# Kernel tuning notes

Measured on AMD Instinct MI355X. Metric: run time of the kernel, lower is better.

## Reference

```python
import jax, jax.numpy as jnp
import numpy as np

B, N = 2, 6
H, W = 64, 64            # BEV grid
FH, FW = 32, 88          # camera feature map
DIM, FEAT_DIM = 128, 128
HEADS, DH = 4, 32
QW1, QW2 = 8, 8          # query window
KW1, KW2 = 4, 11         # key/val window
IMG_H, IMG_W = 224, 480
EPS = 1e-5


def _ln(t, g, b):
    m = t.mean(-1, keepdims=True)
    v = ((t - m) ** 2).mean(-1, keepdims=True)
    return (t - m) / jnp.sqrt(v + EPS) * g + b


def _bn_relu_conv(t, g, b, Wc):
    # eval-mode BatchNorm2d (running_mean=0, running_var=1) -> ReLU -> 1x1 conv
    y = jax.nn.relu(t / jnp.sqrt(1.0 + EPS) * g[:, None, None] + b[:, None, None])
    return jnp.einsum('oc,nchw->nohw', Wc, y)


def _normalize(t, axis):
    n = jnp.sqrt(jnp.sum(t * t, axis=axis, keepdims=True))
    return t / jnp.maximum(n, 1e-12)


def _win(t, w1, w2):
    # (..., X*w1, Y*w2, d) -> (..., X, Y, w1, w2, d)
    s = t.shape
    t = t.reshape(*s[:-3], s[-3] // w1, w1, s[-2] // w2, w2, s[-1])
    return jnp.swapaxes(t, -4, -3)


def _unwin(t):
    # (..., X, Y, w1, w2, d) -> (..., X*w1, Y*w2, d)
    s = t.shape
    return jnp.swapaxes(t, -4, -3).reshape(*s[:-5], s[-5] * s[-3], s[-4] * s[-2], s[-1])


def _gridwin(t, w1, w2):
    bb, nn, Ht, Wt, d = t.shape
    t = t.reshape(bb, nn, w1, Ht // w1, w2, Wt // w2, d)
    return t.transpose(0, 1, 3, 5, 2, 4, 6)  # (b, n, X, Y, w1, w2, d)


def _cross_win_attn(qw, kw, vw, ln_g, ln_b, Wqkv, bqkv, Wp, bp, skip):
    b, n, X, Y, w1, w2, d = qw.shape
    f1, f2 = kw.shape[4], kw.shape[5]
    L = X * Y
    q = qw.transpose(0, 2, 3, 1, 4, 5, 6).reshape(b, L, n * w1 * w2, d)
    k = kw.transpose(0, 2, 3, 1, 4, 5, 6).reshape(b, L, n * f1 * f2, d)
    v = vw.transpose(0, 2, 3, 1, 4, 5, 6).reshape(b, L, n * f1 * f2, d)
    q = _ln(q, ln_g[0], ln_b[0]) @ Wqkv[0] + bqkv[0]
    k = _ln(k, ln_g[1], ln_b[1]) @ Wqkv[1] + bqkv[1]
    v = _ln(v, ln_g[2], ln_b[2]) @ Wqkv[2] + bqkv[2]
    split = lambda t: t.reshape(*t.shape[:-1], HEADS, DH)  # head-major channel split
    q, k, v = split(q), split(k), split(v)
    att = jax.nn.softmax(DH ** -0.5 * jnp.einsum('blqhd,blkhd->bhlqk', q, k), axis=-1)
    o = jnp.einsum('bhlqk,blkhd->blqhd', att, v).reshape(b, L, n * w1 * w2, HEADS * DH)
    o = o @ Wp + bp
    o = o.reshape(b, X, Y, n, w1, w2, d).mean(3)  # mean over cameras
    return o + skip


def _forward(x, grid, feature, I_inv, E_inv,
             bn_fl_g, bn_fl_b, W_fl, bn_fp_g, bn_fp_b, W_fp,
             W_bev, b_bev, W_img, W_cam,
             attn_ln_g, attn_ln_b, attn_Wqkv, attn_bqkv, attn_Wp, attn_bp,
             pn_g, pn_b, Wma, bma, Wmb, bmb, post_g, post_b):
    b, n = feature.shape[:2]
    # image plane (buffer)
    xs = jnp.linspace(0.0, 1.0, FW) * IMG_W
    ys = jnp.linspace(0.0, 1.0, FH) * IMG_H
    gx, gy = jnp.meshgrid(xs, ys)  # (FH, FW) each
    plane = jnp.stack([gx, gy, jnp.ones_like(gx)], 0).reshape(3, FH * FW)
    # camera embedding from translation column of E_inv
    c = E_inv[..., -1]                                   # (b, n, 4)
    c_embed = jnp.einsum('oc,bnc->bno', W_cam, c)        # (b, n, dim)
    # unprojected rays
    cam = jnp.einsum('bnij,jk->bnik', I_inv, plane)      # (b, n, 3, HW)
    cam = jnp.concatenate([cam, jnp.ones_like(cam[:, :, :1])], 2)
    d = jnp.einsum('bnij,bnjk->bnik', E_inv, cam)        # (b, n, 4, HW)
    d_img = d.reshape(b, n, 4, FH, FW)
    d_embed = jnp.einsum('oc,bnchw->bnohw', W_img, d_img)
    img_embed = _normalize(d_embed - c_embed[..., None, None], axis=2)
    # BEV positional embedding
    w_embed = jnp.einsum('oc,chw->ohw', W_bev, grid[:2]) + b_bev[:, None, None]
    bev_embed = _normalize(w_embed[None, None] - c_embed[..., None, None], axis=2)  # (b,n,dim,H,W)
    feat = feature.reshape(b * n, FEAT_DIM, FH, FW)
    key_im = img_embed + _bn_relu_conv(feat, bn_fp_g, bn_fp_b, W_fp).reshape(b, n, DIM, FH, FW)
    val_im = _bn_relu_conv(feat, bn_fl_g, bn_fl_b, W_fl).reshape(b, n, DIM, FH, FW)
    query = bev_embed + x[:, None]                       # (b, n, dim, H, W)
    # channel-last
    q_im = query.transpose(0, 1, 3, 4, 2)
    k_im = key_im.transpose(0, 1, 3, 4, 2)
    v_im = val_im.transpose(0, 1, 3, 4, 2)
    x_im = x.transpose(0, 2, 3, 1)
    # stage 1: local windows
    qw = _win(q_im, QW1, QW2)
    kw = _win(k_im, KW1, KW2)
    vw = _win(v_im, KW1, KW2)
    o1 = _cross_win_attn(qw, kw, vw, attn_ln_g[0], attn_ln_b[0], attn_Wqkv[0],
                         attn_bqkv[0], attn_Wp[0], attn_bp[0], _win(x_im, QW1, QW2))
    q1 = _unwin(o1)                                      # (b, H, W, d)
    q1 = q1 + jax.nn.gelu(_ln(q1, pn_g[0], pn_b[0]) @ Wma[0] + bma[0], approximate=False) @ Wmb[0] + bmb[0]
    # stage 2: grid (swapped) windows
    qg = jnp.broadcast_to(q1[:, None], (b, n) + q1.shape[1:])
    o2 = _cross_win_attn(_win(qg, QW1, QW2), _gridwin(k_im, KW1, KW2), _gridwin(v_im, KW1, KW2),
                         attn_ln_g[1], attn_ln_b[1], attn_Wqkv[1], attn_bqkv[1],
                         attn_Wp[1], attn_bp[1], _win(q1, QW1, QW2))
    q2 = _unwin(o2)
    q2 = q2 + jax.nn.gelu(_ln(q2, pn_g[1], pn_b[1]) @ Wma[1] + bma[1], approximate=False) @ Wmb[1] + bmb[1]
    out = _ln(q2, post_g, post_b)
    return out.transpose(0, 3, 1, 2)                     # (b, dim, H, W)


def setup_inputs() -> dict:
    key = jax.random.key(0)
    ks = jax.random.split(key, 16)
    rn = lambda i, shape, sc=0.02: jax.random.normal(ks[i], shape, dtype=jnp.float32) * sc
    return {
        'index': 0,
        'x': jax.random.normal(ks[0], (B, DIM, H, W), dtype=jnp.float32),
        'grid': jax.random.normal(ks[1], (2, H, W), dtype=jnp.float32),
        'feature': jax.random.normal(ks[2], (B, N, FEAT_DIM, FH, FW), dtype=jnp.float32),
        'I_inv': jax.random.normal(ks[3], (B, N, 3, 3), dtype=jnp.float32),
        'E_inv': jax.random.normal(ks[4], (B, N, 4, 4), dtype=jnp.float32),
        'bn_fl_g': jnp.ones((FEAT_DIM,), jnp.float32), 'bn_fl_b': jnp.zeros((FEAT_DIM,), jnp.float32),
        'W_fl': rn(5, (DIM, FEAT_DIM)),
        'bn_fp_g': jnp.ones((FEAT_DIM,), jnp.float32), 'bn_fp_b': jnp.zeros((FEAT_DIM,), jnp.float32),
        'W_fp': rn(6, (DIM, FEAT_DIM)),
        'W_bev': rn(7, (DIM, 2)), 'b_bev': jnp.zeros((DIM,), jnp.float32),
        'W_img': rn(8, (DIM, 4)), 'W_cam': rn(9, (DIM, 4)),
        'attn_ln_g': jnp.ones((2, 3, DIM), jnp.float32), 'attn_ln_b': jnp.zeros((2, 3, DIM), jnp.float32),
        'attn_Wqkv': rn(10, (2, 3, DIM, HEADS * DH)), 'attn_bqkv': jnp.zeros((2, 3, HEADS * DH), jnp.float32),
        'attn_Wp': rn(11, (2, HEADS * DH, DIM)), 'attn_bp': jnp.zeros((2, DIM), jnp.float32),
        'pn_g': jnp.ones((2, DIM), jnp.float32), 'pn_b': jnp.zeros((2, DIM), jnp.float32),
        'Wma': rn(12, (2, DIM, 2 * DIM)), 'bma': jnp.zeros((2, 2 * DIM), jnp.float32),
        'Wmb': rn(13, (2, 2 * DIM, DIM)), 'bmb': jnp.zeros((2, DIM), jnp.float32),
        'post_g': jnp.ones((DIM,), jnp.float32), 'post_b': jnp.zeros((DIM,), jnp.float32),
    }


def reference(index, x, grid, feature, I_inv, E_inv,
              bn_fl_g, bn_fl_b, W_fl, bn_fp_g, bn_fp_b, W_fp,
              W_bev, b_bev, W_img, W_cam,
              attn_ln_g, attn_ln_b, attn_Wqkv, attn_bqkv, attn_Wp, attn_bp,
              pn_g, pn_b, Wma, bma, Wmb, bmb, post_g, post_b):
    del index  # grid for this index is passed directly
    return _forward(x, grid, feature, I_inv, E_inv,
                    bn_fl_g, bn_fl_b, W_fl, bn_fp_g, bn_fp_b, W_fp,
                    W_bev, b_bev, W_img, W_cam,
                    attn_ln_g, attn_ln_b, attn_Wqkv, attn_bqkv, attn_Wp, attn_bp,
                    pn_g, pn_b, Wma, bma, Wmb, bmb, post_g, post_b)
```

## Files before the change

### kernel.cpp

```cpp
#include <hip/hip_runtime.h>
#include <math.h>


typedef __attribute__((ext_vector_type(8))) short short8;
typedef __attribute__((ext_vector_type(4))) float f32x4;

__device__ __forceinline__ unsigned short f2bf(float f){
  union { float f; unsigned u; } v; v.f = f;
  unsigned r = v.u + 0x7FFF + ((v.u >> 16) & 1);
  return (unsigned short)(r >> 16);
}
__device__ __forceinline__ float bf2f(unsigned short h){
  union { unsigned u; float f; } v; v.u = ((unsigned)h) << 16; return v.f;
}
__device__ __forceinline__ void store_bf16x8(unsigned short* p, const float* v){
  union { short8 s8; unsigned short u[8]; } u;
  #pragma unroll
  for (int i=0;i<8;i++) u.u[i] = f2bf(v[i]);
  *(short8*)p = u.s8;
}

__device__ __forceinline__ float gelu_erf(float x){
  float z = x * 0.70710678118654752f;
  float a = fabsf(z);
  float t = 1.0f / fmaf(0.3275911f, a, 1.0f);
  float p = t*(0.254829592f + t*(-0.284496736f + t*(1.421413741f +
            t*(-1.453152027f + t*1.061405429f))));
  float er = 1.0f - p*__expf(-a*a);
  er = copysignf(er, z);
  return 0.5f * x * (1.0f + er);
}

__device__ __forceinline__ size_t remap_kv(int tok, int mode){
  int bn = tok / 2816; int p = tok - bn*2816;
  int b = bn / 6, n = bn - b*6;
  int i = p / 88, j = p - i*88;
  int l, t;
  if (mode == 1){
    int jw = j / 11;
    l = (i >> 2)*8 + jw;
    t = n*44 + (i & 3)*11 + (j - jw*11);
  } else {
    l = (i & 7)*8 + (j & 7);
    t = n*44 + (i >> 3)*11 + (j >> 3);
  }
  return (size_t)((b*64 + l)*264 + t);
}

__global__ __launch_bounds__(128) void k_prep(
    const float* __restrict__ qkv, const float* __restrict__ wp,
    const float* __restrict__ wma, const float* __restrict__ wmb,
    const float* __restrict__ wfl, const float* __restrict__ wfp,
    unsigned short* __restrict__ Wt,
    const float* __restrict__ Iinv, const float* __restrict__ Einv,
    const float* __restrict__ Wimg, const float* __restrict__ Wcam,
    unsigned short* __restrict__ K1h,
    const float* __restrict__ gridp, const float* __restrict__ Wbev,
    const float* __restrict__ bbev, const float* __restrict__ x,
    const float* __restrict__ lg, const float* __restrict__ lb,
    unsigned short* __restrict__ Qh){
  __shared__ float sx[128][9];
  int bid = blockIdx.x;
  if (bid < 64){
    const int sel[16]  = {0,0,0,0,0,0, 1,1, 2,2, 3,3,3,3, 4,5};
    const int soff[16] = {0,16384,32768,49152,65536,81920, 0,16384, 0,32768,
                          0,16384,32768,49152, 0,0};
    const int doff[16] = {0,16384,32768,49152,65536,81920, 98304,114688,
                          131072,163840, 196608,212992,229376,245760, 262144,278528};
    const int Ns[16]   = {128,128,128,128,128,128, 128,128, 256,256,
                          128,128,128,128, 128,128};
    const int trs[16]  = {1,1,1,1,1,1, 1,1, 1,1, 1,1,1,1, 0,0};
    int sg = bid >> 2, q = bid & 3;
    const float* srcs[6] = {qkv, wp, wma, wmb, wfl, wfp};
    const float* src = srcs[sel[sg]] + soff[sg];
    unsigned short* dst = Wt + doff[sg];
    int K = 128, N = Ns[sg];
    int quarter = (K*N) >> 2;
    for (int idx = q*quarter + threadIdx.x; idx < (q+1)*quarter; idx += 128){
      int n = idx / K, k = idx - n*K;
      float v = trs[sg] ? src[k*N + n] : src[idx];
      dst[idx] = f2bf(v);
    }
  } else if (bid < 4288){
    int tile = bid - 64;
    int bn = tile / 352; int p0 = (tile - bn*352)*8;
    int xid = threadIdx.x >> 4, part = threadIdx.x & 15;
    int p = p0 + xid;
    int i = p / 88, j = p - i*88;
    float xs = (float)j * (480.0f/87.0f);
    float ys = (float)i * (224.0f/31.0f);
    const float* I = Iinv + bn*9;
    const float* E = Einv + bn*16;
    float c0 = I[0]*xs + I[1]*ys + I[2];
    float c1 = I[3]*xs + I[4]*ys + I[5];
    float c2 = I[6]*xs + I[7]*ys + I[8];
    float d0 = E[0]*c0 + E[1]*c1 + E[2]*c2 + E[3];
    float d1 = E[4]*c0 + E[5]*c1 + E[6]*c2 + E[7];
    float d2 = E[8]*c0 + E[9]*c1 + E[10]*c2 + E[11];
    float d3 = E[12]*c0 + E[13]*c1 + E[14]*c2 + E[15];
    float v[8]; float sq = 0.f;
    #pragma unroll
    for (int k=0;k<8;k++){
      int o = part*8 + k;
      const float* W = Wimg + o*4;
      const float* Wc = Wcam + o*4;
      float de = W[0]*d0 + W[1]*d1 + W[2]*d2 + W[3]*d3;
      float ce = Wc[0]*E[3] + Wc[1]*E[7] + Wc[2]*E[11] + Wc[3]*E[15];
      float vv = de - ce;
      v[k] = vv; sq = fmaf(vv, vv, sq);
    }
    #pragma unroll
    for (int off=8; off>0; off>>=1) sq += __shfl_xor(sq, off, 16);
    float rn = 1.0f / fmaxf(sqrtf(sq), 1e-12f);
    float o8[8];
    #pragma unroll
    for (int k=0;k<8;k++) o8[k] = v[k]*rn;
    store_bf16x8(K1h + (size_t)(bn*2816 + p)*128 + part*8, o8);
  } else {
    int bid2 = bid - 4288;
    int b = bid2 >> 9; int pp0 = (bid2 & 511) << 3;
    {
      int cg = threadIdx.x >> 3, px = threadIdx.x & 7;
      #pragma unroll
      for (int i=0;i<8;i++){
        int c = cg + 16*i;
        sx[c][px] = x[(size_t)b*524288 + (size_t)c*4096 + pp0 + px];
      }
    }
    __syncthreads();
    int xid = threadIdx.x >> 4, part = threadIdx.x & 15;
    int pix = pp0 + xid;
    int h = pix >> 6, w = pix & 63;
    int l = (h>>3)*8 + (w>>3);
    int tq = (h&7)*8 + (w&7);
    float g0 = gridp[pix], g1 = gridp[4096 + pix];
    float we[8], xv[8];
    #pragma unroll
    for (int k=0;k<8;k++){
      int o = part*8 + k;
      we[k] = Wbev[o*2]*g0 + Wbev[o*2+1]*g1 + bbev[o];
      xv[k] = sx[part*8+k][xid];
    }
    for (int n=0; n<6; n++){
      const float* E = Einv + (b*6+n)*16;
      float v[8]; float sq = 0.f;
      #pragma unroll
      for (int k=0;k<8;k++){
        int o = part*8 + k;
        const float* Wc = Wcam + o*4;
        float ce = Wc[0]*E[3] + Wc[1]*E[7] + Wc[2]*E[11] + Wc[3]*E[15];
        float vv = we[k] - ce;
        v[k] = vv; sq = fmaf(vv, vv, sq);
      }
      #pragma unroll
      for (int off=8; off>0; off>>=1) sq += __shfl_xor(sq, off, 16);
      float rn = 1.0f / fmaxf(sqrtf(sq), 1e-12f);
      float q[8]; float s=0.f, s2=0.f;
      #pragma unroll
      for (int k=0;k<8;k++){
        q[k] = fmaf(v[k], rn, xv[k]);
        s += q[k]; s2 = fmaf(q[k], q[k], s2);
      }
      #pragma unroll
      for (int off=8; off>0; off>>=1){ s += __shfl_xor(s, off, 16); s2 += __shfl_xor(s2, off, 16); }
      float mean = s*(1.f/128.f);
      float rstd = rsqrtf(fmaxf(s2*(1.f/128.f) - mean*mean, 0.f) + 1e-5f);
      size_t row = (size_t)((b*64 + l)*384 + n*64 + tq);
      float o8[8];
      #pragma unroll
      for (int k=0;k<8;k++){
        int c = part*8 + k;
        o8[k] = fmaf((q[k]-mean)*rstd, lg[c], lb[c]);
      }
      store_bf16x8(Qh + row*128 + part*8, o8);
    }
  }
}

struct GArg {
  const unsigned short* Xh; const float* Xf; int ldx;
  const float* lg; const float* lb;
  const unsigned short* Wt; const float* bias;
  unsigned short* OUTH; int ldout; float oscale;
  int do_ln; int outmode; int conv;
};

template<int MT>
__global__ __launch_bounds__(256) void k_gemm3(GArg ga, GArg gb, GArg gc,
                                               int s1, int s2){
  constexpr int KP_ = 136;
  constexpr int MTILES = MT / 16;
  constexpr int TPR = 256 / MT;
  constexpr int KPT = 128 / TPR;
  __shared__ unsigned short sW[128*KP_];
  __shared__ unsigned short sA[MT*KP_];
  __shared__ float sg[128], sb[128], sbias[128];
  const int b0 = (int)blockIdx.x;
  const GArg g = (b0 < s1) ? ga : (b0 < s2) ? gb : gc;
  const int bid = (b0 < s1) ? b0 : (b0 < s2) ? b0 - s1 : b0 - s2;
  const int base = bid * MT;
  const int tid = threadIdx.x;
  for (int i = tid; i < 2048; i += 256){
    int n = i >> 4, k8 = (i & 15) << 3;
    *(short8*)&sW[n*KP_ + k8] = *(const short8*)(g.Wt + (size_t)n*128 + k8);
  }
  if (tid < 128){
    if (g.do_ln || g.conv){ sg[tid]=g.lg[tid]; sb[tid]=g.lb[tid]; }
    sbias[tid] = g.bias ? g.bias[tid] : 0.f;
  }
  const float RSQ = rsqrtf(1.0f + 1e-5f);
  if (g.conv){
    int prow = tid & 63, cseg = tid >> 6;
    int bn = base / 2816;
    int p = base - bn*2816 + prow;
    const float* fb = g.Xf + ((size_t)bn*128 + cseg*32)*2816 + p;
    #pragma unroll
    for (int i=0;i<32;i+=2){
      int c = cseg*32 + i;
      float t0 = fb[(size_t)i*2816] * RSQ;
      float t1 = fb[(size_t)(i+1)*2816] * RSQ;
      float y0 = fmaxf(fmaf(t0, sg[c],   sb[c]),   0.f);
      float y1 = fmaxf(fmaf(t1, sg[c+1], sb[c+1]), 0.f);
      unsigned u = (unsigned)f2bf(y0) | ((unsigned)f2bf(y1) << 16);
      *(unsigned*)&sA[prow*KP_ + c] = u;
    }
  } else {
    const int r = tid / TPR, part = tid % TPR;
    unsigned short* dst = sA + r*KP_ + part*KPT;
    float v[KPT];
    if (g.Xf){
      const float* src = g.Xf + (size_t)(base+r)*g.ldx + part*KPT;
      #pragma unroll
      for (int k=0;k<KPT;k+=4){
        float4 t = *(const float4*)(src + k);
        v[k]=t.x; v[k+1]=t.y; v[k+2]=t.z; v[k+3]=t.w;
      }
    } else {
      const unsigned short* src = g.Xh + (size_t)(base+r)*g.ldx + part*KPT;
      #pragma unroll
      for (int k=0;k<KPT;k+=8){
        union { short8 s; unsigned short u[8]; } t;
        t.s = *(const short8*)(src+k);
        #pragma unroll
        for (int i2=0;i2<8;i2++) v[k+i2] = bf2f(t.u[i2]);
      }
    }
    if (g.do_ln){
      float s=0.f, s2=0.f;
      #pragma unroll
      for (int k=0;k<KPT;k++){ s += v[k]; s2 = fmaf(v[k],v[k],s2); }
      #pragma unroll
      for (int off=TPR/2; off>0; off>>=1){
        s += __shfl_xor(s, off, TPR); s2 += __shfl_xor(s2, off, TPR);
      }
      float mean = s * (1.f/128.f);
      float rstd = rsqrtf(fmaxf(s2*(1.f/128.f) - mean*mean, 0.f) + 1e-5f);
      #pragma unroll
      for (int k=0;k<KPT;k++){
        int c = part*KPT + k;
        v[k] = fmaf((v[k]-mean)*rstd, sg[c], sb[c]);
      }
    }
    #pragma unroll
    for (int k=0;k<KPT;k+=8) store_bf16x8(dst+k, v+k);
  }
  __syncthreads();
  const int lane = tid & 63, wv = tid >> 6;
  const int lane15 = lane & 15, quad = lane >> 4;
  const int n0 = wv * 32;
  f32x4 acc[MTILES][2];
  #pragma unroll
  for (int mt=0; mt<MTILES; mt++){ acc[mt][0]=(f32x4)0.f; acc[mt][1]=(f32x4)0.f; }
  const unsigned short* aptr = sA + lane15*KP_ + quad*8;
  const unsigned short* bptr = sW + (size_t)(n0 + lane15)*KP_ + quad*8;
  #pragma unroll
  for (int kk=0; kk<4; kk++){
    short8 af[MTILES], bf2v[2];
    #pragma unroll
    for (int mt=0; mt<MTILES; mt++) af[mt] = *(const short8*)(aptr + mt*16*KP_ + kk*32);
    bf2v[0] = *(const short8*)(bptr + kk*32);
    bf2v[1] = *(const short8*)(bptr + 16*KP_ + kk*32);
    #pragma unroll
    for (int mt=0; mt<MTILES; mt++){
      acc[mt][0] = __builtin_amdgcn_mfma_f32_16x16x32_bf16(af[mt], bf2v[0], acc[mt][0], 0,0,0);
      acc[mt][1] = __builtin_amdgcn_mfma_f32_16x16x32_bf16(af[mt], bf2v[1], acc[mt][1], 0,0,0);
    }
  }
  __syncthreads();
  #pragma unroll
  for (int mt=0; mt<MTILES; mt++){
    #pragma unroll
    for (int nt=0; nt<2; nt++){
      int col = n0 + nt*16 + lane15;
      float bsv = sbias[col];
      #pragma unroll
      for (int r4=0; r4<4; r4++){
        int row = mt*16 + quad*4 + r4;
        float v = (acc[mt][nt][r4] + bsv) * g.oscale;
        if (g.outmode == 3)
          v += bf2f(g.OUTH[(size_t)(base+row)*g.ldout + col]);
        sA[row*KP_ + col] = f2bf(v);
      }
    }
  }
  __syncthreads();
  for (int i = tid; i < MT*16; i += 256){
    int row = i >> 4, seg = i & 15;
    int rrow = base + row;
    size_t orow = (g.outmode==1||g.outmode==2) ? remap_kv(rrow, g.outmode) : (size_t)rrow;
    *(short8*)(g.OUTH + orow*(size_t)g.ldout + seg*8) = *(const short8*)&sA[row*KP_ + seg*8];
  }
}

__global__ __launch_bounds__(256) void k_tail(
    const unsigned short* __restrict__ AOh,
    const float* __restrict__ skipf, int skipmode,
    const unsigned short* __restrict__ WtP, const float* __restrict__ abp,
    const float* __restrict__ png, const float* __restrict__ pnb,
    const unsigned short* __restrict__ WtMAa, const unsigned short* __restrict__ WtMAb,
    const float* __restrict__ bma,
    const unsigned short* __restrict__ WtMBa, const unsigned short* __restrict__ WtMBb,
    const float* __restrict__ bmb,
    float* __restrict__ Q1out,
    const float* __restrict__ postg, const float* __restrict__ postb,
    float* __restrict__ out){
  constexpr int KP_ = 136;
  __shared__ unsigned short sW[128*KP_];
  __shared__ unsigned short sX[32*KP_];
  __shared__ unsigned short sH1[32*KP_];
  __shared__ unsigned short sH2[32*KP_];
  __shared__ float sCUR[32*132];
  __shared__ float sbias[128];
  __shared__ float sg[128], sb2[128];
  __shared__ float sMean[32], sRstd[32];
  const int tid = threadIdx.x;
  const int base = blockIdx.x * 32;
  const int lane = tid & 63, wv = tid >> 6;
  const int lane15 = lane & 15, quad = lane >> 4;
  const int n0 = wv * 32;

  auto loadW = [&](const unsigned short* Wp){
    for (int i = tid; i < 2048; i += 256){
      int n = i >> 4, k8 = (i & 15) << 3;
      *(short8*)&sW[n*KP_ + k8] = *(const short8*)(Wp + (size_t)n*128 + k8);
    }
  };
  auto domfma = [&](const unsigned short* Asrc, f32x4 acc[2][2]){
    const unsigned short* aptr = Asrc + lane15*KP_ + quad*8;
    const unsigned short* bptr = sW + (size_t)(n0 + lane15)*KP_ + quad*8;
    #pragma unroll
    for (int kk=0; kk<4; kk++){
      short8 a0 = *(const short8*)(aptr + kk*32);
      short8 a1 = *(const short8*)(aptr + 16*KP_ + kk*32);
      short8 b0 = *(const short8*)(bptr + kk*32);
      short8 b1 = *(const short8*)(bptr + 16*KP_ + kk*32);
      acc[0][0] = __builtin_amdgcn_mfma_f32_16x16x32_bf16(a0,b0,acc[0][0],0,0,0);
      acc[1][0] = __builtin_amdgcn_mfma_f32_16x16x32_bf16(a1,b0,acc[1][0],0,0,0);
      acc[0][1] = __builtin_amdgcn_mfma_f32_16x16x32_bf16(a0,b1,acc[0][1],0,0,0);
      acc[1][1] = __builtin_amdgcn_mfma_f32_16x16x32_bf16(a1,b1,acc[1][1],0,0,0);
    }
  };

  loadW(WtP);
  {
    const int r = tid >> 3, part = tid & 7;
    const short8* src = (const short8*)(AOh + (size_t)(base+r)*128 + part*16);
    short8* dst = (short8*)(sX + r*KP_ + part*16);
    dst[0] = src[0]; dst[1] = src[1];
  }
  if (tid < 128){ sbias[tid] = abp[tid]; sg[tid] = png[tid]; sb2[tid] = pnb[tid]; }
  __syncthreads();
  {
    f32x4 acc[2][2];
    acc[0][0]=(f32x4)0.f; acc[0][1]=(f32x4)0.f;
    acc[1][0]=(f32x4)0.f; acc[1][1]=(f32x4)0.f;
    domfma(sX, acc);
    #pragma unroll
    for (int mt=0; mt<2; mt++)
      #pragma unroll
      for (int nt=0; nt<2; nt++){
        int col = n0 + nt*16 + lane15;
        float bsv = sbias[col];
        #pragma unroll
        for (int r4=0; r4<4; r4++){
          int row = mt*16 + quad*4 + r4;
          int rrow = base + row;
          float v = acc[mt][nt][r4] + bsv;
          if (skipmode == 1){
            int bb = rrow >> 12, l = (rrow >> 6) & 63, pp = rrow & 63;
            int pix = (((l>>3)*8 + (pp>>3)) << 6) + (l&7)*8 + (pp&7);
            v += skipf[(size_t)bb*524288 + (size_t)col*4096 + pix];
          } else {
            v += skipf[(size_t)rrow*128 + col];
          }
          sCUR[row*132 + col] = v;
        }
      }
  }
  __syncthreads();
  loadW(WtMAa);
  if (tid < 128) sbias[tid] = bma[tid];
  {
    const int r = tid >> 3, part = tid & 7;
    float v[16];
    #pragma unroll
    for (int k=0;k<16;k++) v[k] = sCUR[r*132 + part*16 + k];
    float s=0.f, s2=0.f;
    #pragma unroll
    for (int k=0;k<16;k++){ s += v[k]; s2 = fmaf(v[k],v[k],s2); }
    #pragma unroll
    for (int off=4; off>0; off>>=1){ s += __shfl_xor(s, off, 8); s2 += __shfl_xor(s2, off, 8); }
    float mean = s*(1.f/128.f);
    float rstd = rsqrtf(fmaxf(s2*(1.f/128.f) - mean*mean, 0.f) + 1e-5f);
    #pragma unroll
    for (int k=0;k<16;k++){
      int c = part*16 + k;
      v[k] = fmaf((v[k]-mean)*rstd, sg[c], sb2[c]);
    }
    store_bf16x8(sX + r*KP_ + part*16, v);
    store_bf16x8(sX + r*KP_ + part*16 + 8, v+8);
  }
  __syncthreads();
  {
    f32x4 acc[2][2];
    acc[0][0]=(f32x4)0.f; acc[0][1]=(f32x4)0.f;
    acc[1][0]=(f32x4)0.f; acc[1][1]=(f32x4)0.f;
    domfma(sX, acc);
    #pragma unroll
    for (int mt=0; mt<2; mt++)
      #pragma unroll
      for (int nt=0; nt<2; nt++){
        int col = n0 + nt*16 + lane15;
        float bsv = sbias[col];
        #pragma unroll
        for (int r4=0; r4<4; r4++){
          int row = mt*16 + quad*4 + r4;
          sH1[row*KP_ + col] = f2bf(gelu_erf(acc[mt][nt][r4] + bsv));
        }
      }
  }
  __syncthreads();
  loadW(WtMAb);
  if (tid < 128) sbias[tid] = bma[128 + tid];
  __syncthreads();
  {
    f32x4 acc[2][2];
    acc[0][0]=(f32x4)0.f; acc[0][1]=(f32x4)0.f;
    acc[1][0]=(f32x4)0.f; acc[1][1]=(f32x4)0.f;
    domfma(sX, acc);
    #pragma unroll
    for (int mt=0; mt<2; mt++)
      #pragma unroll
      for (int nt=0; nt<2; nt++){
        int col = n0 + nt*16 + lane15;
        float bsv = sbias[col];
        #pragma unroll
        for (int r4=0; r4<4; r4++){
          int row = mt*16 + quad*4 + r4;
          sH2[row*KP_ + col] = f2bf(gelu_erf(acc[mt][nt][r4] + bsv));
        }
      }
  }
  __syncthreads();
  loadW(WtMBa);
  if (tid < 128) sbias[tid] = bmb[tid];
  __syncthreads();
  f32x4 acc[2][2];
  acc[0][0]=(f32x4)0.f; acc[0][1]=(f32x4)0.f;
  acc[1][0]=(f32x4)0.f; acc[1][1]=(f32x4)0.f;
  domfma(sH1, acc);
  __syncthreads();
  loadW(WtMBb);
  __syncthreads();
  domfma(sH2, acc);
  if (out == nullptr){
    #pragma unroll
    for (int mt=0; mt<2; mt++)
      #pragma unroll
      for (int nt=0; nt<2; nt++){
        int col = n0 + nt*16 + lane15;
        float bsv = sbias[col];
        #pragma unroll
        for (int r4=0; r4<4; r4++){
          int row = mt*16 + quad*4 + r4;
          Q1out[(size_t)(base+row)*128 + col] = acc[mt][nt][r4] + bsv + sCUR[row*132 + col];
        }
      }
  } else {
    float res[2][2][4];
    #pragma unroll
    for (int mt=0; mt<2; mt++)
      #pragma unroll
      for (int nt=0; nt<2; nt++){
        int col = n0 + nt*16 + lane15;
        float bsv = sbias[col];
        #pragma unroll
        for (int r4=0; r4<4; r4++){
          int row = mt*16 + quad*4 + r4;
          res[mt][nt][r4] = acc[mt][nt][r4] + bsv + sCUR[row*132 + col];
        }
      }
    __syncthreads();
    #pragma unroll
    for (int mt=0; mt<2; mt++)
      #pragma unroll
      for (int nt=0; nt<2; nt++){
        int col = n0 + nt*16 + lane15;
        #pragma unroll
        for (int r4=0; r4<4; r4++){
          int row = mt*16 + quad*4 + r4;
          sCUR[row*132 + col] = res[mt][nt][r4];
        }
      }
    __syncthreads();
    {
      const int r = tid >> 3, part = tid & 7;
      float v[16];
      #pragma unroll
      for (int k=0;k<16;k++) v[k] = sCUR[r*132 + part*16 + k];
      float s=0.f, s2=0.f;
      #pragma unroll
      for (int k=0;k<16;k++){ s += v[k]; s2 = fmaf(v[k],v[k],s2); }
      #pragma unroll
      for (int off=4; off>0; off>>=1){ s += __shfl_xor(s, off, 8); s2 += __shfl_xor(s2, off, 8); }
      if (part == 0){
        float mean = s*(1.f/128.f);
        sMean[r] = mean;
        sRstd[r] = rsqrtf(fmaxf(s2*(1.f/128.f) - mean*mean, 0.f) + 1e-5f);
      }
    }
    __syncthreads();
    {
      int c = tid & 127, half = tid >> 7;
      int b = base >> 12, l = (base >> 6) & 63, p0 = base & 63;
      float go = postg[c], bo = postb[c];
      #pragma unroll
      for (int seg=0; seg<2; seg++){
        int p = p0 + half*16 + seg*8;
        int hrow = (l>>3)*8 + (p>>3);
        int w0 = (l&7)*8;
        float rr[8];
        #pragma unroll
        for (int j=0;j<8;j++){
          int row = half*16 + seg*8 + j;
          rr[j] = fmaf((sCUR[row*132 + c] - sMean[row])*sRstd[row], go, bo);
        }
        size_t obase = ((size_t)(b*128 + c))*4096 + (size_t)hrow*64 + w0;
        *(float4*)&out[obase]   = make_float4(rr[0],rr[1],rr[2],rr[3]);
        *(float4*)&out[obase+4] = make_float4(rr[4],rr[5],rr[6],rr[7]);
      }
    }
  }
}

__global__ __launch_bounds__(256) void k_attn2(const unsigned short* __restrict__ QPh,
    const unsigned short* __restrict__ KPh, const unsigned short* __restrict__ VPh,
    unsigned short* __restrict__ AOh, int nrep, int nQ){
  __shared__ unsigned short Ksh[288*40];
  __shared__ unsigned short Vt[32*296];
  __shared__ unsigned short Psh[4*16*40];
  __shared__ float rs[4*16];
  int hd = blockIdx.x & 3; int bl = blockIdx.x >> 2;
  size_t kvbase = (size_t)bl*264;
  int tid = threadIdx.x;
  for (int idx = tid; idx < 1056; idx += 256){
    int row = idx >> 2, seg = idx & 3;
    *(short8*)&Ksh[row*40 + seg*8] =
      *(const short8*)(KPh + (kvbase+row)*128 + hd*32 + seg*8);
  }
  for (int idx = tid; idx < 96; idx += 256){
    int row = 264 + (idx>>2), seg = idx & 3;
    short8 z = {0,0,0,0,0,0,0,0};
    *(short8*)&Ksh[row*40 + seg*8] = z;
  }
  for (int idx = tid; idx < 1056; idx += 256){
    int row = idx >> 2, seg = idx & 3;
    union { short8 s; unsigned short u[8]; } t;
    t.s = *(const short8*)(VPh + (kvbase+row)*128 + hd*32 + seg*8);
    #pragma unroll
    for (int i=0;i<8;i++) Vt[(seg*8+i)*296 + row] = t.u[i];
  }
  for (int idx = tid; idx < 384; idx += 256){
    int d = idx / 12, kp = 264 + (idx % 12)*2;
    *(unsigned*)&Vt[d*296 + kp] = 0u;
  }
  __syncthreads();
  const int wv = tid >> 6, lane = tid & 63;
  const int lane15 = lane & 15, quad = lane >> 4;
  unsigned short* Pw = Psh + wv*640;
  float* rsw = rs + wv*16;
  short8 vfrag[9][2];
  #pragma unroll
  for (int kc=0; kc<9; kc++){
    vfrag[kc][0] = *(const short8*)&Vt[(lane15)*296      + kc*32 + quad*8];
    vfrag[kc][1] = *(const short8*)&Vt[(16+lane15)*296   + kc*32 + quad*8];
  }
  f32x4 macc0 = (f32x4)0.f, macc1 = (f32x4)0.f;
  for (int cam = 0; cam < nrep; cam++){
    int qrow = bl*nQ + (cam*4 + wv)*16 + lane15;
    short8 qf = *(const short8*)(QPh + (size_t)qrow*128 + hd*32 + quad*8);
    f32x4 oa0 = (f32x4)0.f, oa1 = (f32x4)0.f;
    float rsum = 0.f;
    #pragma unroll
    for (int kc=0; kc<9; kc++){
      #pragma unroll
      for (int sub=0; sub<2; sub++){
        int kt = kc*2 + sub;
        short8 kf = *(const short8*)&Ksh[(kt*16 + lane15)*40 + quad*8];
        f32x4 st = __builtin_amdgcn_mfma_f32_16x16x32_bf16(kf, qf, (f32x4)0.f, 0,0,0);
        int kbase = kt*16 + quad*4;
        float e0 = (kbase+0 < 264) ? __expf(st[0]) : 0.f;
        float e1 = (kbase+1 < 264) ? __expf(st[1]) : 0.f;
        float e2 = (kbase+2 < 264) ? __expf(st[2]) : 0.f;
        float e3 = (kbase+3 < 264) ? __expf(st[3]) : 0.f;
        rsum += (e0+e1)+(e2+e3);
        uint2 pk;
        pk.x = (unsigned)f2bf(e0) | ((unsigned)f2bf(e1) << 16);
        pk.y = (unsigned)f2bf(e2) | ((unsigned)f2bf(e3) << 16);
        *(uint2*)&Pw[lane15*40 + sub*16 + quad*4] = pk;
      }
      short8 pf = *(const short8*)&Pw[lane15*40 + quad*8];
      oa0 = __builtin_amdgcn_mfma_f32_16x16x32_bf16(pf, vfrag[kc][0], oa0, 0,0,0);
      oa1 = __builtin_amdgcn_mfma_f32_16x16x32_bf16(pf, vfrag[kc][1], oa1, 0,0,0);
    }
    rsum += __shfl_xor(rsum, 16);
    rsum += __shfl_xor(rsum, 32);
    if (lane < 16) rsw[lane] = rsum;
    f32x4 rv = *(f32x4*)&rsw[quad*4];
    #pragma unroll
    for (int r=0;r<4;r++){
      float inv = 1.f / rv[r];
      macc0[r] = fmaf(oa0[r], inv, macc0[r]);
      macc1[r] = fmaf(oa1[r], inv, macc1[r]);
    }
  }
  float sc = (nrep == 6) ? (1.f/6.f) : 1.f;
  int pixb = wv*16 + quad*4;
  #pragma unroll
  for (int r=0;r<4;r++){
    size_t rowo = ((size_t)(bl*64 + pixb + r))*128 + hd*32;
    AOh[rowo + lane15]      = f2bf(macc0[r]*sc);
    AOh[rowo + 16 + lane15] = f2bf(macc1[r]*sc);
  }
}

extern "C" void kernel_launch(void* const* d_in, const int* in_sizes, int n_in,
                              void* d_out, int out_size, void* d_ws, size_t ws_size,
                              hipStream_t stream) {
  (void)in_sizes; (void)n_in; (void)out_size; (void)ws_size;
  const float* x     = (const float*)d_in[1];
  const float* gridp = (const float*)d_in[2];
  const float* feat  = (const float*)d_in[3];
  const float* Iinv  = (const float*)d_in[4];
  const float* Einv  = (const float*)d_in[5];
  const float* gfl   = (const float*)d_in[6];
  const float* bfl   = (const float*)d_in[7];
  const float* Wfl   = (const float*)d_in[8];
  const float* gfp   = (const float*)d_in[9];
  const float* bfp   = (const float*)d_in[10];
  const float* Wfp   = (const float*)d_in[11];
  const float* Wbev  = (const float*)d_in[12];
  const float* bbev  = (const float*)d_in[13];
  const float* Wimg  = (const float*)d_in[14];
  const float* Wcam  = (const float*)d_in[15];
  const float* alng  = (const float*)d_in[16];
  const float* alnb  = (const float*)d_in[17];
  const float* aWqkv = (const float*)d_in[18];
  const float* abqkv = (const float*)d_in[19];
  const float* aWp   = (const float*)d_in[20];
  const float* abp   = (const float*)d_in[21];
  const float* png   = (const float*)d_in[22];
  const float* pnb   = (const float*)d_in[23];
  const float* Wma   = (const float*)d_in[24];
  const float* bma   = (const float*)d_in[25];
  const float* Wmb   = (const float*)d_in[26];
  const float* bmb   = (const float*)d_in[27];
  const float* postg = (const float*)d_in[28];
  const float* postb = (const float*)d_in[29];
  float* out = (float*)d_out;
  float* ws  = (float*)d_ws;
  const float QSC = 0.17677669529663687f;

  unsigned short* Wt  = (unsigned short*)(ws + 2048);
  unsigned short* K1h = (unsigned short*)(ws + 149504);
  unsigned short* V1h = K1h + 4325376;
  unsigned short* KPh = V1h + 4325376;
  unsigned short* VPh = KPh + 4325376;
  unsigned short* QPh = VPh + 4325376;
  unsigned short* Qbh = QPh + 6291456;
  unsigned short* AOh = Qbh + 6291456;
  float* Q1f = (float*)(AOh + 1048576);

  unsigned short* WtQ1 = Wt;            unsigned short* WtK1 = Wt + 16384;
  unsigned short* WtV1 = Wt + 32768;    unsigned short* WtQ2 = Wt + 49152;
  unsigned short* WtK2 = Wt + 65536;    unsigned short* WtV2 = Wt + 81920;
  unsigned short* WtP1 = Wt + 98304;    unsigned short* WtP2 = Wt + 114688;
  unsigned short* WtMA1 = Wt + 131072;  unsigned short* WtMA2 = Wt + 163840;
  unsigned short* WtMB1a = Wt + 196608; unsigned short* WtMB1b = Wt + 212992;
  unsigned short* WtMB2a = Wt + 229376; unsigned short* WtMB2b = Wt + 245760;
  unsigned short* WtFL = Wt + 262144;   unsigned short* WtFP = Wt + 278528;

  GArg Z{}; Z.oscale = 1.f;

  k_prep<<<5312, 128, 0, stream>>>(aWqkv, aWp, Wma, Wmb, Wfl, Wfp, Wt,
      Iinv, Einv, Wimg, Wcam, K1h, gridp, Wbev, bbev, x, alng, alnb, Qbh);

  {
    GArg ck = Z, cv = Z;
    ck.Xf = feat; ck.conv = 1; ck.lg = gfp; ck.lb = bfp; ck.Wt = WtFP;
    ck.OUTH = K1h; ck.ldout = 128; ck.outmode = 3;
    cv = ck; cv.lg = gfl; cv.lb = bfl; cv.Wt = WtFL; cv.OUTH = V1h;
    cv.outmode = 0;
    k_gemm3<64><<<1056, 256, 0, stream>>>(ck, cv, cv, 528, 1056);
  }
  {
    GArg q = Z, kk = Z, vv = Z;
    q.Xh = Qbh; q.ldx = 128; q.Wt = WtQ1; q.bias = abqkv; q.OUTH = QPh;
    q.ldout = 128; q.oscale = QSC;
    kk.Xh = K1h; kk.ldx = 128; kk.do_ln = 1; kk.lg = alng+128; kk.lb = alnb+128;
    kk.Wt = WtK1; kk.bias = abqkv+128; kk.OUTH = KPh; kk.ldout = 128;
    kk.outmode = 1;
    vv = kk; vv.Xh = V1h; vv.lg = alng+256; vv.lb = alnb+256; vv.Wt = WtV1;
    vv.bias = abqkv+256; vv.OUTH = VPh;
    k_gemm3<64><<<1824, 256, 0, stream>>>(q, kk, vv, 768, 1296);
  }
  k_attn2<<<512, 256, 0, stream>>>(QPh, KPh, VPh, AOh, 6, 384);
  k_tail<<<256, 256, 0, stream>>>(AOh, x, 1, WtP1, abp, png, pnb,
      WtMA1, WtMA1+16384, bma, WtMB1a, WtMB1b, bmb, Q1f,
      nullptr, nullptr, nullptr);
  {
    GArg q = Z, kk = Z, vv = Z;
    q.Xf = Q1f; q.ldx = 128; q.do_ln = 1; q.lg = alng+384; q.lb = alnb+384;
    q.Wt = WtQ2; q.bias = abqkv+384; q.OUTH = QPh; q.ldout = 128;
    q.oscale = QSC;
    kk.Xh = K1h; kk.ldx = 128; kk.do_ln = 1; kk.lg = alng+512; kk.lb = alnb+512;
    kk.Wt = WtK2; kk.bias = abqkv+512; kk.OUTH = KPh; kk.ldout = 128;
    kk.outmode = 2;
    vv = kk; vv.Xh = V1h; vv.lg = alng+640; vv.lb = alnb+640; vv.Wt = WtV2;
    vv.bias = abqkv+640; vv.OUTH = VPh;
    k_gemm3<64><<<1184, 256, 0, stream>>>(q, kk, vv, 128, 656);
  }
  k_attn2<<<512, 256, 0, stream>>>(QPh, KPh, VPh, AOh, 1, 64);
  k_tail<<<256, 256, 0, stream>>>(AOh, Q1f, 3, WtP2, abp+128, png+128, pnb+128,
      WtMA2, WtMA2+16384, bma+256, WtMB2a, WtMB2b, bmb+128, nullptr,
      postg, postb, out);
}
```

Baseline: 274.5 us.

## Fold LayerNorm affine into QKV weights and precompute normalized K/V/Q inputs

The LayerNorm gamma is folded into the QKV projection weights and the beta into precomputed biases. The conv kernel now applies the plain normalization once and stores normalized K1/V1, and the first tail kernel emits a normalized bf16 copy of Q1. The QKV GEMMs therefore become plain bf16 copies plus MFMA with 128-row tiles and no per-row LN. The aim is to avoid recomputing LN twice per K/V set and to halve the block count. The cost is extra bf16 rounding of normalized values and fewer, larger blocks.

Result: no change. 279.0 us (+1.6%).

```diff
diff --git a/kernel.cpp b/kernel.cpp
--- a/kernel.cpp
+++ b/kernel.cpp
@@ -58,6 +58,7 @@
     const float* __restrict__ gridp, const float* __restrict__ Wbev,
     const float* __restrict__ bbev, const float* __restrict__ x,
     const float* __restrict__ lg, const float* __restrict__ lb,
+    const float* __restrict__ abqkv, float* __restrict__ biasP,
     unsigned short* __restrict__ Qh){
   __shared__ float sx[128][9];
   int bid = blockIdx.x;
@@ -76,13 +77,26 @@
     unsigned short* dst = Wt + doff[sg];
     int K = 128, N = Ns[sg];
     int quarter = (K*N) >> 2;
+    bool fold = (sg >= 1 && sg <= 5);
+    const float* gv = lg + sg*128;
     for (int idx = q*quarter + threadIdx.x; idx < (q+1)*quarter; idx += 128){
       int n = idx / K, k = idx - n*K;
       float v = trs[sg] ? src[k*N + n] : src[idx];
+      if (fold) v *= gv[k];
       dst[idx] = f2bf(v);
     }
-  } else if (bid < 4288){
-    int tile = bid - 64;
+  } else if (bid < 70){
+    int m = bid - 64;
+    int n = threadIdx.x;
+    float s = abqkv[m*128 + n];
+    if (m > 0){
+      const float* lnb = lb + m*128;
+      const float* W = qkv + m*16384;
+      for (int k=0;k<128;k++) s = fmaf(lnb[k], W[k*128 + n], s);
+    }
+    biasP[m*128 + n] = s;
+  } else if (bid < 4294){
+    int tile = bid - 70;
     int bn = tile / 352; int p0 = (tile - bn*352)*8;
     int xid = threadIdx.x >> 4, part = threadIdx.x & 15;
     int p = p0 + xid;
@@ -117,7 +131,7 @@
     for (int k=0;k<8;k++) o8[k] = v[k]*rn;
     store_bf16x8(K1h + (size_t)(bn*2816 + p)*128 + part*8, o8);
   } else {
-    int bid2 = bid - 4288;
+    int bid2 = bid - 4294;
     int b = bid2 >> 9; int pp0 = (bid2 & 511) << 3;
     {
       int cg = threadIdx.x >> 3, px = threadIdx.x & 7;
@@ -177,46 +191,38 @@
   }
 }
 
-struct GArg {
-  const unsigned short* Xh; const float* Xf; int ldx;
-  const float* lg; const float* lb;
-  const unsigned short* Wt; const float* bias;
-  unsigned short* OUTH; int ldout; float oscale;
-  int do_ln; int outmode; int conv;
-};
-
-template<int MT>
-__global__ __launch_bounds__(256) void k_gemm3(GArg ga, GArg gb, GArg gc,
-                                               int s1, int s2){
+__global__ __launch_bounds__(256) void k_conv(const float* __restrict__ feat,
+    const float* __restrict__ gK, const float* __restrict__ bK,
+    const unsigned short* __restrict__ WK, unsigned short* __restrict__ K1h,
+    const float* __restrict__ gV, const float* __restrict__ bV,
+    const unsigned short* __restrict__ WV, unsigned short* __restrict__ V1h){
   constexpr int KP_ = 136;
-  constexpr int MTILES = MT / 16;
-  constexpr int TPR = 256 / MT;
-  constexpr int KPT = 128 / TPR;
   __shared__ unsigned short sW[128*KP_];
-  __shared__ unsigned short sA[MT*KP_];
-  __shared__ float sg[128], sb[128], sbias[128];
-  const int b0 = (int)blockIdx.x;
-  const GArg g = (b0 < s1) ? ga : (b0 < s2) ? gb : gc;
-  const int bid = (b0 < s1) ? b0 : (b0 < s2) ? b0 - s1 : b0 - s2;
-  const int base = bid * MT;
+  __shared__ unsigned short sA[128*KP_];
+  __shared__ float sg[128], sb[128];
+  __shared__ float sMean[128], sRstd[128];
+  const int which = (blockIdx.x >= 264);
+  const int bid = which ? blockIdx.x - 264 : blockIdx.x;
+  const float* gg = which ? gV : gK;
+  const float* bb = which ? bV : bK;
+  const unsigned short* Wts = which ? WV : WK;
+  unsigned short* OUT = which ? V1h : K1h;
   const int tid = threadIdx.x;
+  const int base = bid * 128;
   for (int i = tid; i < 2048; i += 256){
     int n = i >> 4, k8 = (i & 15) << 3;
-    *(short8*)&sW[n*KP_ + k8] = *(const short8*)(g.Wt + (size_t)n*128 + k8);
-  }
-  if (tid < 128){
-    if (g.do_ln || g.conv){ sg[tid]=g.lg[tid]; sb[tid]=g.lb[tid]; }
-    sbias[tid] = g.bias ? g.bias[tid] : 0.f;
-  }
+    *(short8*)&sW[n*KP_ + k8] = *(const short8*)(Wts + (size_t)n*128 + k8);
+  }
+  if (tid < 128){ sg[tid]=gg[tid]; sb[tid]=bb[tid]; }
   const float RSQ = rsqrtf(1.0f + 1e-5f);
-  if (g.conv){
-    int prow = tid & 63, cseg = tid >> 6;
+  {
+    int prow = tid & 127, cseg = tid >> 7;
     int bn = base / 2816;
     int p = base - bn*2816 + prow;
-    const float* fb = g.Xf + ((size_t)bn*128 + cseg*32)*2816 + p;
-    #pragma unroll
-    for (int i=0;i<32;i+=2){
-      int c = cseg*32 + i;
+    const float* fb = feat + ((size_t)bn*128 + cseg*64)*2816 + p;
+    #pragma unroll 8
+    for (int i=0;i<64;i+=2){
+      int c = cseg*64 + i;
       float t0 = fb[(size_t)i*2816] * RSQ;
       float t1 = fb[(size_t)(i+1)*2816] * RSQ;
       float y0 = fmaxf(fmaf(t0, sg[c],   sb[c]),   0.f);
@@ -224,71 +230,127 @@
       unsigned u = (unsigned)f2bf(y0) | ((unsigned)f2bf(y1) << 16);
       *(unsigned*)&sA[prow*KP_ + c] = u;
     }
-  } else {
-    const int r = tid / TPR, part = tid % TPR;
-    unsigned short* dst = sA + r*KP_ + part*KPT;
-    float v[KPT];
-    if (g.Xf){
-      const float* src = g.Xf + (size_t)(base+r)*g.ldx + part*KPT;
-      #pragma unroll
-      for (int k=0;k<KPT;k+=4){
-        float4 t = *(const float4*)(src + k);
-        v[k]=t.x; v[k+1]=t.y; v[k+2]=t.z; v[k+3]=t.w;
-      }
-    } else {
-      const unsigned short* src = g.Xh + (size_t)(base+r)*g.ldx + part*KPT;
-      #pragma unroll
-      for (int k=0;k<KPT;k+=8){
-        union { short8 s; unsigned short u[8]; } t;
-        t.s = *(const short8*)(src+k);
-        #pragma unroll
-        for (int i2=0;i2<8;i2++) v[k+i2] = bf2f(t.u[i2]);
-      }
-    }
-    if (g.do_ln){
-      float s=0.f, s2=0.f;
-      #pragma unroll
-      for (int k=0;k<KPT;k++){ s += v[k]; s2 = fmaf(v[k],v[k],s2); }
-      #pragma unroll
-      for (int off=TPR/2; off>0; off>>=1){
-        s += __shfl_xor(s, off, TPR); s2 += __shfl_xor(s2, off, TPR);
-      }
-      float mean = s * (1.f/128.f);
-      float rstd = rsqrtf(fmaxf(s2*(1.f/128.f) - mean*mean, 0.f) + 1e-5f);
-      #pragma unroll
-      for (int k=0;k<KPT;k++){
-        int c = part*KPT + k;
-        v[k] = fmaf((v[k]-mean)*rstd, sg[c], sb[c]);
-      }
-    }
-    #pragma unroll
-    for (int k=0;k<KPT;k+=8) store_bf16x8(dst+k, v+k);
   }
   __syncthreads();
   const int lane = tid & 63, wv = tid >> 6;
   const int lane15 = lane & 15, quad = lane >> 4;
   const int n0 = wv * 32;
-  f32x4 acc[MTILES][2];
+  f32x4 acc[8][2];
   #pragma unroll
-  for (int mt=0; mt<MTILES; mt++){ acc[mt][0]=(f32x4)0.f; acc[mt][1]=(f32x4)0.f; }
+  for (int mt=0; mt<8; mt++){ acc[mt][0]=(f32x4)0.f; acc[mt][1]=(f32x4)0.f; }
   const unsigned short* aptr = sA + lane15*KP_ + quad*8;
   const unsigned short* bptr = sW + (size_t)(n0 + lane15)*KP_ + quad*8;
   #pragma unroll
   for (int kk=0; kk<4; kk++){
-    short8 af[MTILES], bf2v[2];
-    #pragma unroll
-    for (int mt=0; mt<MTILES; mt++) af[mt] = *(const short8*)(aptr + mt*16*KP_ + kk*32);
+    short8 af[8], bf2v[2];
+    #pragma unroll
+    for (int mt=0; mt<8; mt++) af[mt] = *(const short8*)(aptr + mt*16*KP_ + kk*32);
     bf2v[0] = *(const short8*)(bptr + kk*32);
     bf2v[1] = *(const short8*)(bptr + 16*KP_ + kk*32);
     #pragma unroll
-    for (int mt=0; mt<MTILES; mt++){
+    for (int mt=0; mt<8; mt++){
       acc[mt][0] = __builtin_amdgcn_mfma_f32_16x16x32_bf16(af[mt], bf2v[0], acc[mt][0], 0,0,0);
       acc[mt][1] = __builtin_amdgcn_mfma_f32_16x16x32_bf16(af[mt], bf2v[1], acc[mt][1], 0,0,0);
     }
   }
   __syncthreads();
   #pragma unroll
-  for (int mt=0; mt<MTILES; mt++){
+  for (int mt=0; mt<8; mt++){
+    #pragma unroll
+    for (int nt=0; nt<2; nt++){
+      int col = n0 + nt*16 + lane15;
+      #pragma unroll
+      for (int r4=0; r4<4; r4++){
+        int row = mt*16 + quad*4 + r4;
+        float v = acc[mt][nt][r4];
+        if (!which) v += bf2f(K1h[(size_t)(base+row)*128 + col]);
+        sA[row*KP_ + col] = f2bf(v);
+      }
+    }
+  }
+  __syncthreads();
+  {
+    int r = tid >> 1, part = tid & 1;
+    float s=0.f, s2=0.f;
+    #pragma unroll 8
+    for (int k=0;k<64;k++){
+      float v = bf2f(sA[r*KP_ + part*64 + k]);
+      s += v; s2 = fmaf(v,v,s2);
+    }
+    s += __shfl_xor(s, 1); s2 += __shfl_xor(s2, 1);
+    if (part == 0){
+      float mean = s*(1.f/128.f);
+      sMean[r] = mean;
+      sRstd[r] = rsqrtf(fmaxf(s2*(1.f/128.f) - mean*mean, 0.f) + 1e-5f);
+    }
+  }
+  __syncthreads();
+  for (int i = tid; i < 2048; i += 256){
+    int row = i >> 4, seg = i & 15;
+    float mean = sMean[row], rstd = sRstd[row];
+    union { short8 s; unsigned short u[8]; } t;
+    t.s = *(const short8*)&sA[row*KP_ + seg*8];
+    float v[8];
+    #pragma unroll
+    for (int k=0;k<8;k++) v[k] = (bf2f(t.u[k]) - mean)*rstd;
+    store_bf16x8(OUT + (size_t)(base+row)*128 + seg*8, v);
+  }
+}
+
+struct GArg {
+  const unsigned short* Xh;
+  const unsigned short* Wt; const float* bias;
+  unsigned short* OUTH; float oscale; int outmode;
+};
+
+__global__ __launch_bounds__(256) void k_qkv(GArg ga, GArg gb, GArg gc,
+                                             int s1, int s2){
+  constexpr int KP_ = 136;
+  __shared__ unsigned short sW[128*KP_];
+  __shared__ unsigned short sA[128*KP_];
+  __shared__ float sbias[128];
+  const int b0 = (int)blockIdx.x;
+  const GArg g = (b0 < s1) ? ga : (b0 < s2) ? gb : gc;
+  const int bid = (b0 < s1) ? b0 : (b0 < s2) ? b0 - s1 : b0 - s2;
+  const int base = bid * 128;
+  const int tid = threadIdx.x;
+  for (int i = tid; i < 2048; i += 256){
+    int n = i >> 4, k8 = (i & 15) << 3;
+    *(short8*)&sW[n*KP_ + k8] = *(const short8*)(g.Wt + (size_t)n*128 + k8);
+  }
+  if (tid < 128) sbias[tid] = g.bias[tid];
+  {
+    const int r = tid >> 1, part = tid & 1;
+    const short8* src = (const short8*)(g.Xh + (size_t)(base+r)*128 + part*64);
+    short8* dst = (short8*)(sA + r*KP_ + part*64);
+    #pragma unroll
+    for (int k=0;k<8;k++) dst[k] = src[k];
+  }
+  __syncthreads();
+  const int lane = tid & 63, wv = tid >> 6;
+  const int lane15 = lane & 15, quad = lane >> 4;
+  const int n0 = wv * 32;
+  f32x4 acc[8][2];
+  #pragma unroll
+  for (int mt=0; mt<8; mt++){ acc[mt][0]=(f32x4)0.f; acc[mt][1]=(f32x4)0.f; }
+  const unsigned short* aptr = sA + lane15*KP_ + quad*8;
+  const unsigned short* bptr = sW + (size_t)(n0 + lane15)*KP_ + quad*8;
+  #pragma unroll
+  for (int kk=0; kk<4; kk++){
+    short8 af[8], bf2v[2];
+    #pragma unroll
+    for (int mt=0; mt<8; mt++) af[mt] = *(const short8*)(aptr + mt*16*KP_ + kk*32);
+    bf2v[0] = *(const short8*)(bptr + kk*32);
+    bf2v[1] = *(const short8*)(bptr + 16*KP_ + kk*32);
+    #pragma unroll
+    for (int mt=0; mt<8; mt++){
+      acc[mt][0] = __builtin_amdgcn_mfma_f32_16x16x32_bf16(af[mt], bf2v[0], acc[mt][0], 0,0,0);
+      acc[mt][1] = __builtin_amdgcn_mfma_f32_16x16x32_bf16(af[mt], bf2v[1], acc[mt][1], 0,0,0);
+    }
+  }
+  __syncthreads();
+  #pragma unroll
+  for (int mt=0; mt<8; mt++){
     #pragma unroll
     for (int nt=0; nt<2; nt++){
       int col = n0 + nt*16 + lane15;
@@ -296,19 +358,16 @@
       #pragma unroll
       for (int r4=0; r4<4; r4++){
         int row = mt*16 + quad*4 + r4;
-        float v = (acc[mt][nt][r4] + bsv) * g.oscale;
-        if (g.outmode == 3)
-          v += bf2f(g.OUTH[(size_t)(base+row)*g.ldout + col]);
-        sA[row*KP_ + col] = f2bf(v);
-      }
-    }
-  }
-  __syncthreads();
-  for (int i = tid; i < MT*16; i += 256){
+        sA[row*KP_ + col] = f2bf((acc[mt][nt][r4] + bsv) * g.oscale);
+      }
+    }
+  }
+  __syncthreads();
+  for (int i = tid; i < 2048; i += 256){
     int row = i >> 4, seg = i & 15;
     int rrow = base + row;
-    size_t orow = (g.outmode==1||g.outmode==2) ? remap_kv(rrow, g.outmode) : (size_t)rrow;
-    *(short8*)(g.OUTH + orow*(size_t)g.ldout + seg*8) = *(const short8*)&sA[row*KP_ + seg*8];
+    size_t orow = g.outmode ? remap_kv(rrow, g.outmode) : (size_t)rrow;
+    *(short8*)(g.OUTH + orow*128 + seg*8) = *(const short8*)&sA[row*KP_ + seg*8];
   }
 }
 
@@ -321,7 +380,7 @@
     const float* __restrict__ bma,
     const unsigned short* __restrict__ WtMBa, const unsigned short* __restrict__ WtMBb,
     const float* __restrict__ bmb,
-    float* __restrict__ Q1out,
+    float* __restrict__ Q1out, unsigned short* __restrict__ Q1n,
     const float* __restrict__ postg, const float* __restrict__ postb,
     float* __restrict__ out){
   constexpr int KP_ = 136;
@@ -483,9 +542,37 @@
         #pragma unroll
         for (int r4=0; r4<4; r4++){
           int row = mt*16 + quad*4 + r4;
-          Q1out[(size_t)(base+row)*128 + col] = acc[mt][nt][r4] + bsv + sCUR[row*132 + col];
+          float v = acc[mt][nt][r4] + bsv + sCUR[row*132 + col];
+          sCUR[row*132 + col] = v;
+          Q1out[(size_t)(base+row)*128 + col] = v;
         }
       }
+    __syncthreads();
+    {
+      const int r = tid >> 3, part = tid & 7;
+      float s=0.f, s2=0.f;
+      #pragma unroll
+      for (int k=0;k<16;k++){
+        float v = sCUR[r*132 + part*16 + k];
+        s += v; s2 = fmaf(v,v,s2);
+      }
+      #pragma unroll
+      for (int off=4; off>0; off>>=1){ s += __shfl_xor(s, off, 8); s2 += __shfl_xor(s2, off, 8); }
+      if (part == 0){
+        float mean = s*(1.f/128.f);
+        sMean[r] = mean;
+        sRstd[r] = rsqrtf(fmaxf(s2*(1.f/128.f) - mean*mean, 0.f) + 1e-5f);
+      }
+    }
+    __syncthreads();
+    for (int i = tid; i < 512; i += 256){
+      int row = i >> 4, seg = i & 15;
+      float mean = sMean[row], rstd = sRstd[row];
+      float v[8];
+      #pragma unroll
+      for (int k=0;k<8;k++) v[k] = (sCUR[row*132 + seg*8 + k] - mean)*rstd;
+      store_bf16x8(Q1n + (size_t)(base+row)*128 + seg*8, v);
+    }
   } else {
     float res[2][2][4];
     #pragma unroll
@@ -515,12 +602,12 @@
     __syncthreads();
     {
       const int r = tid >> 3, part = tid & 7;
-      float v[16];
-      #pragma unroll
-      for (int k=0;k<16;k++) v[k] = sCUR[r*132 + part*16 + k];
       float s=0.f, s2=0.f;
       #pragma unroll
-      for (int k=0;k<16;k++){ s += v[k]; s2 = fmaf(v[k],v[k],s2); }
+      for (int k=0;k<16;k++){
+        float v = sCUR[r*132 + part*16 + k];
+        s += v; s2 = fmaf(v,v,s2);
+      }
       #pragma unroll
       for (int off=4; off>0; off>>=1){ s += __shfl_xor(s, off, 8); s2 += __shfl_xor(s2, off, 8); }
       if (part == 0){
@@ -681,6 +768,7 @@
   float* ws  = (float*)d_ws;
   const float QSC = 0.17677669529663687f;
 
+  float* biasP = ws;
   unsigned short* Wt  = (unsigned short*)(ws + 2048);
   unsigned short* K1h = (unsigned short*)(ws + 149504);
   unsigned short* V1h = K1h + 4325376;
@@ -690,6 +778,7 @@
   unsigned short* Qbh = QPh + 6291456;
   unsigned short* AOh = Qbh + 6291456;
   float* Q1f = (float*)(AOh + 1048576);
+  unsigned short* Q1n = (unsigned short*)(Q1f + 1048576);
 
   unsigned short* WtQ1 = Wt;            unsigned short* WtK1 = Wt + 16384;
   unsigned short* WtV1 = Wt + 32768;    unsigned short* WtQ2 = Wt + 49152;
@@ -700,48 +789,31 @@
   unsigned short* WtMB2a = Wt + 229376; unsigned short* WtMB2b = Wt + 245760;
   unsigned short* WtFL = Wt + 262144;   unsigned short* WtFP = Wt + 278528;
 
-  GArg Z{}; Z.oscale = 1.f;
-
-  k_prep<<<5312, 128, 0, stream>>>(aWqkv, aWp, Wma, Wmb, Wfl, Wfp, Wt,
-      Iinv, Einv, Wimg, Wcam, K1h, gridp, Wbev, bbev, x, alng, alnb, Qbh);
-
-  {
-    GArg ck = Z, cv = Z;
-    ck.Xf = feat; ck.conv = 1; ck.lg = gfp; ck.lb = bfp; ck.Wt = WtFP;
-    ck.OUTH = K1h; ck.ldout = 128; ck.outmode = 3;
-    cv = ck; cv.lg = gfl; cv.lb = bfl; cv.Wt = WtFL; cv.OUTH = V1h;
-    cv.outmode = 0;
-    k_gemm3<64><<<1056, 256, 0, stream>>>(ck, cv, cv, 528, 1056);
-  }
-  {
-    GArg q = Z, kk = Z, vv = Z;
-    q.Xh = Qbh; q.ldx = 128; q.Wt = WtQ1; q.bias = abqkv; q.OUTH = QPh;
-    q.ldout = 128; q.oscale = QSC;
-    kk.Xh = K1h; kk.ldx = 128; kk.do_ln = 1; kk.lg = alng+128; kk.lb = alnb+128;
-    kk.Wt = WtK1; kk.bias = abqkv+128; kk.OUTH = KPh; kk.ldout = 128;
-    kk.outmode = 1;
-    vv = kk; vv.Xh = V1h; vv.lg = alng+256; vv.lb = alnb+256; vv.Wt = WtV1;
-    vv.bias = abqkv+256; vv.OUTH = VPh;
-    k_gemm3<64><<<1824, 256, 0, stream>>>(q, kk, vv, 768, 1296);
+  k_prep<<<5318, 128, 0, stream>>>(aWqkv, aWp, Wma, Wmb, Wfl, Wfp, Wt,
+      Iinv, Einv, Wimg, Wcam, K1h, gridp, Wbev, bbev, x, alng, alnb,
+      abqkv, biasP, Qbh);
+
+  k_conv<<<528, 256, 0, stream>>>(feat, gfp, bfp, WtFP, K1h,
+                                  gfl, bfl, WtFL, V1h);
+
+  {
+    GArg q{Qbh, WtQ1, biasP,      QPh, QSC, 0};
+    GArg kk{K1h, WtK1, biasP+128, KPh, 1.f, 1};
+    GArg vv{V1h, WtV1, biasP+256, VPh, 1.f, 1};
+    k_qkv<<<912, 256, 0, stream>>>(q, kk, vv, 384, 648);
   }
   k_attn2<<<512, 256, 0, stream>>>(QPh, KPh, VPh, AOh, 6, 384);
   k_tail<<<256, 256, 0, stream>>>(AOh, x, 1, WtP1, abp, png, pnb,
-      WtMA1, WtMA1+16384, bma, WtMB1a, WtMB1b, bmb, Q1f,
+      WtMA1, WtMA1+16384, bma, WtMB1a, WtMB1b, bmb, Q1f, Q1n,
       nullptr, nullptr, nullptr);
   {
-    GArg q = Z, kk = Z, vv = Z;
-    q.Xf = Q1f; q.ldx = 128; q.do_ln = 1; q.lg = alng+384; q.lb = alnb+384;
-    q.Wt = WtQ2; q.bias = abqkv+384; q.OUTH = QPh; q.ldout = 128;
-    q.oscale = QSC;
-    kk.Xh = K1h; kk.ldx = 128; kk.do_ln = 1; kk.lg = alng+512; kk.lb = alnb+512;
-    kk.Wt = WtK2; kk.bias = abqkv+512; kk.OUTH = KPh; kk.ldout = 128;
-    kk.outmode = 2;
-    vv = kk; vv.Xh = V1h; vv.lg = alng+640; vv.lb = alnb+640; vv.Wt = WtV2;
-    vv.bias = abqkv+640; vv.OUTH = VPh;
-    k_gemm3<64><<<1184, 256, 0, stream>>>(q, kk, vv, 128, 656);
+    GArg q{Q1n, WtQ2, biasP+384,  QPh, QSC, 0};
+    GArg kk{K1h, WtK2, biasP+512, KPh, 1.f, 2};
+    GArg vv{V1h, WtV2, biasP+640, VPh, 1.f, 2};
+    k_qkv<<<592, 256, 0, stream>>>(q, kk, vv, 64, 328);
   }
   k_attn2<<<512, 256, 0, stream>>>(QPh, KPh, VPh, AOh, 1, 64);
   k_tail<<<256, 256, 0, stream>>>(AOh, Q1f, 3, WtP2, abp+128, png+128, pnb+128,
-      WtMA2, WtMA2+16384, bma+256, WtMB2a, WtMB2b, bmb+128, nullptr,
+      WtMA2, WtMA2+16384, bma+256, WtMB2a, WtMB2b, bmb+128, nullptr, nullptr,
       postg, postb, out);
 }
```
